# Kernel optimization log

Hardware: AMD Instinct MI355X
Metric: run time of the kernel (lower is better)

The kernel has to match this reference:

```python
import jax, jax.numpy as jnp
import numpy as np
from jax import lax

B, C, H, W = 2, 64, 48, 48
NH, DK, DV = 8, 64, 128          # heads, per-head d_k, per-head d_v
DN, NS, R = 128, 16, 4           # SS2D d_inner (expand=2), d_state, dt_rank
MULT = 4                          # FFN expansion
L = H * W


def layer_norm(x, w, b, eps=1e-5):
    m = x.mean(-1, keepdims=True)
    v = ((x - m) ** 2).mean(-1, keepdims=True)
    return (x - m) / jnp.sqrt(v + eps) * w + b


def conv2d(x, w, groups=1):
    # x: NCHW, w: OIHW
    return lax.conv_general_dilated(x, w, (1, 1), 'SAME',
                                    dimension_numbers=('NCHW', 'OIHW', 'NCHW'),
                                    feature_group_count=groups)


def setup_inputs() -> dict:
    key = jax.random.key(0)
    ks = jax.random.split(key, 24)
    rn = lambda k, shp, s=0.02: jax.random.normal(k, shp, jnp.float32) * s
    inp = {
        'enc_input': jax.random.normal(ks[0], (B, C, H, W), jnp.float32),
        'slf_attn_snr': jax.random.uniform(ks[1], (B, 1, H, W), jnp.float32),
        # MultiHeadAttention params
        'attn_wq': rn(ks[2], (C, NH * DK)),
        'attn_wk': rn(ks[3], (C, NH * DK)),
        'attn_wv': rn(ks[4], (C, NH * DV)),
        'attn_fc': rn(ks[5], (NH * DV, C)),
        'attn_ln_w': jnp.ones((C,), jnp.float32),
        'attn_ln_b': jnp.zeros((C,), jnp.float32),
        # SS2D params
        'ss_in_w': rn(ks[6], (C, 2 * DN)),
        'ss_conv_w': rn(ks[7], (DN, 1, 3, 3)),
        'ss_conv_b': jnp.zeros((DN,), jnp.float32),
        'ss_xproj_w': rn(ks[8], (4, R + 2 * NS, DN)),
        'ss_dt_w': rn(ks[9], (4, DN, R)),
        'ss_dt_b': rn(ks[10], (4, DN)),
        'ss_Alog': jnp.log(jnp.broadcast_to(jnp.arange(1, NS + 1, dtype=jnp.float32), (4, DN, NS))),
        'ss_D': jnp.ones((4, DN), jnp.float32),
        'ss_norm_w': jnp.ones((DN,), jnp.float32),
        'ss_norm_b': jnp.zeros((DN,), jnp.float32),
        'ss_out_w': rn(ks[11], (DN, C)),
        # FFN (PreNorm + conv block)
        'ffn_ln_w': jnp.ones((C,), jnp.float32),
        'ffn_ln_b': jnp.zeros((C,), jnp.float32),
        'ffn_w1': rn(ks[12], (C * MULT, C, 1, 1)),
        'ffn_dw': rn(ks[13], (C * MULT, 1, 3, 3)),
        'ffn_w2': rn(ks[14], (C, C * MULT, 1, 1)),
    }
    return inp


def reference(enc_input, slf_attn_snr, attn_wq, attn_wk, attn_wv, attn_fc,
              attn_ln_w, attn_ln_b, ss_in_w, ss_conv_w, ss_conv_b, ss_xproj_w,
              ss_dt_w, ss_dt_b, ss_Alog, ss_D, ss_norm_w, ss_norm_b, ss_out_w,
              ffn_ln_w, ffn_ln_b, ffn_w1, ffn_dw, ffn_w2):
    # ---- Multi-head self-attention over spatial tokens (SNR-biased) ----
    x_tok = enc_input.reshape(B, C, L).transpose(0, 2, 1)        # (B, L, C)
    q = (x_tok @ attn_wq).reshape(B, L, NH, DK).transpose(0, 2, 1, 3)
    k = (x_tok @ attn_wk).reshape(B, L, NH, DK).transpose(0, 2, 1, 3)
    v = (x_tok @ attn_wv).reshape(B, L, NH, DV).transpose(0, 2, 1, 3)
    scores = jnp.einsum('bhqd,bhkd->bhqk', q, k) / jnp.sqrt(jnp.float32(DK))
    snr_flat = slf_attn_snr.reshape(B, 1, 1, L)                  # bias over keys
    scores = scores + jnp.log(snr_flat + 1e-4)
    attn = jax.nn.softmax(scores, axis=-1)                       # (B, NH, L, L)
    o = jnp.einsum('bhqk,bhkd->bhqd', attn, v)
    o = o.transpose(0, 2, 1, 3).reshape(B, L, NH * DV) @ attn_fc
    enc_output = layer_norm(o + x_tok, attn_ln_w, attn_ln_b)     # post-LN residual
    enc_output = enc_output.transpose(0, 2, 1).reshape(B, C, H, W)

    # ---- SS2D: 4-direction 2D selective scan ----
    xh = enc_output.transpose(0, 2, 3, 1)                        # (B, H, W, C)
    snr_h = slf_attn_snr.transpose(0, 2, 3, 1)                   # (B, H, W, 1)
    xz = xh @ ss_in_w                                            # (B, H, W, 2*DN)
    x1, z = xz[..., :DN], xz[..., DN:]
    x1 = x1.transpose(0, 3, 1, 2)                                # (B, DN, H, W)
    x1 = conv2d(x1, ss_conv_w, groups=DN) + ss_conv_b[None, :, None, None]
    x1 = jax.nn.silu(x1)

    x_hw = x1.reshape(B, DN, L)
    x_wh = x1.transpose(0, 1, 3, 2).reshape(B, DN, L)
    xs = jnp.stack([x_hw, x_wh], axis=1)                         # (B, 2, DN, L)
    xs = jnp.concatenate([xs, jnp.flip(xs, axis=-1)], axis=1)    # (B, 4, DN, L)

    x_dbl = jnp.einsum('bkdl,kcd->bkcl', xs, ss_xproj_w)
    dts, Bs, Cs = x_dbl[:, :, :R], x_dbl[:, :, R:R + NS], x_dbl[:, :, R + NS:]
    dts = jnp.einsum('bkrl,kdr->bkdl', dts, ss_dt_w) + ss_dt_b[None, :, :, None]
    dts = jax.nn.softplus(dts)                                   # (B, 4, DN, L)
    A = -jnp.exp(ss_Alog)                                        # (4, DN, NS)

    def step(h, inp):
        xt, dtt, Bt, Ct = inp                                    # (B,4,DN),(B,4,DN),(B,4,NS),(B,4,NS)
        dA = jnp.exp(dtt[..., None] * A)                         # (B,4,DN,NS)
        h = h * dA + (dtt * xt)[..., None] * Bt[:, :, None, :]
        y = jnp.einsum('bkdn,bkn->bkd', h, Ct)
        return h, y

    h0 = jnp.zeros((B, 4, DN, NS), jnp.float32)
    elems = (xs.transpose(3, 0, 1, 2), dts.transpose(3, 0, 1, 2),
             Bs.transpose(3, 0, 1, 2), Cs.transpose(3, 0, 1, 2))
    _, ys = lax.scan(step, h0, elems)                            # (L, B, 4, DN)
    ys = ys.transpose(1, 2, 3, 0) + ss_D[None, :, :, None] * xs  # (B, 4, DN, L)

    inv = jnp.flip(ys[:, 2:4], axis=-1)                          # undo reversed scans
    wh = ys[:, 1].reshape(B, DN, W, H).transpose(0, 1, 3, 2).reshape(B, DN, L)
    invwh = inv[:, 1].reshape(B, DN, W, H).transpose(0, 1, 3, 2).reshape(B, DN, L)
    y = ys[:, 0] + inv[:, 0] + wh + invwh                        # (B, DN, L)
    y = y.transpose(0, 2, 1).reshape(B, H, W, DN)
    y = layer_norm(y, ss_norm_w, ss_norm_b) * jax.nn.silu(z) * snr_h
    x2 = y @ ss_out_w + enc_input.transpose(0, 2, 3, 1)          # (B, H, W, C)

    # ---- PreNorm conv FeedForward ----
    xn = layer_norm(x2, ffn_ln_w, ffn_ln_b).transpose(0, 3, 1, 2)
    h1 = jax.nn.gelu(conv2d(xn, ffn_w1), approximate=False)
    h1 = jax.nn.gelu(conv2d(h1, ffn_dw, groups=C * MULT), approximate=False)
    h1 = conv2d(h1, ffn_w2).transpose(0, 2, 3, 1)
    x3 = h1 + x2

    return x3.transpose(0, 3, 1, 2)                              # (B, C, H, W)
```

## Files before the change

### kernel.cpp

```cpp
#include <hip/hip_runtime.h>
#include <hip/hip_bf16.h>

#define Bq 2
#define Cc 64
#define Hh 48
#define Ww 48
#define Ll 2304
#define NHh 8
#define DKk 64
#define DVv 128
#define DNn 128
#define NSs 16
#define Rr 4
#define SCH 48
#define SNC 48
#define TT 8

#define OQ    0u
#define OK_   2359296u
#define OV    4718592u
#define OO    9437184u
#define OX2   15040512u
#define OVT   15630336u
#define WS_NEED_FLOATS (OVT + 4718592u)
#define ODT2  OQ
#define OYS2  OK_
#define OX1P  OV
#define OZ    (OV + 589824u)
#define OX1S  (OV + 1179648u)
#define OBS2  (OV + 1769472u)
#define OCS2  (OV + 2064384u)
#define OCSA  (OV + 2359296u)
#define OCSB  (OV + 3145728u)
#define OHST  (OV + 3932160u)
#define OH1A  OO
#define OH1B  (OO + 1179648u)

typedef short short8v __attribute__((ext_vector_type(8)));
typedef short short4v __attribute__((ext_vector_type(4)));
typedef float f32x4 __attribute__((ext_vector_type(4)));
typedef unsigned short ushort_t;

__device__ __forceinline__ float geluf(float x) {
  return 0.5f * x * (1.0f + erff(x * 0.70710678118654752f));
}
__device__ __forceinline__ float siluf(float x) {
  return x / (1.0f + __expf(-x));
}
__device__ __forceinline__ float softplusf(float x) {
  return fmaxf(x, 0.0f) + log1pf(__expf(-fabsf(x)));
}
__device__ __forceinline__ int spmap(int k, int l) {
  if (k == 0) return l;
  if (k == 1) return (l % 48) * 48 + l / 48;
  if (k == 2) return 2303 - l;
  int l2 = 2303 - l; return (l2 % 48) * 48 + l2 / 48;
}
__device__ __forceinline__ short f2bf(float f) {
  unsigned u = __float_as_uint(f);
  unsigned r = (u + 0x7FFFu + ((u >> 16) & 1u)) >> 16;
  return (short)r;
}

__global__ void k_code(float* out) { if (threadIdx.x == 0) out[0] = 25000.f; }

__global__ __launch_bounds__(256) void k_qkv(const float* __restrict__ enc,
    const float* __restrict__ wq, const float* __restrict__ wk,
    const float* __restrict__ wv, float* __restrict__ ws) {
  int l0 = blockIdx.x * TT; int b = blockIdx.y;
  int t = threadIdx.x;
  __shared__ float xs[64][12];
  {
    int idx = t, c = idx >> 3, i = idx & 7;
    xs[c][i] = enc[(size_t)b * Cc * Ll + (size_t)c * Ll + l0 + i];
    idx = t + 256; c = idx >> 3; i = idx & 7;
    xs[c][i] = enc[(size_t)b * Cc * Ll + (size_t)c * Ll + l0 + i];
  }
  __syncthreads();
  ushort_t* qb = (ushort_t*)(ws + OQ);
  ushort_t* kb = (ushort_t*)(ws + OK_);
  float* v = ws + OV;
#pragma unroll
  for (int g = 0; g < 6; ++g) {
    int j = t + g * 256;
    float acc[TT];
#pragma unroll
    for (int i = 0; i < TT; ++i) acc[i] = 0.f;
    const float* wp; int col, stride;
    if (j < 512) { wp = wq + j; stride = 512; col = j; }
    else if (j < 1024) { wp = wk + (j - 512); stride = 512; col = j - 512; }
    else { wp = wv + (j - 1024); stride = 1024; col = j - 1024; }
    for (int c = 0; c < 64; ++c) {
      float w = wp[(size_t)c * stride];
      const float4* xc = (const float4*)&xs[c][0];
      float4 x0 = xc[0], x1 = xc[1];
      acc[0] += x0.x * w; acc[1] += x0.y * w;
      acc[2] += x0.z * w; acc[3] += x0.w * w;
      acc[4] += x1.x * w; acc[5] += x1.y * w;
      acc[6] += x1.z * w; acc[7] += x1.w * w;
    }
    if (j < 512) {
#pragma unroll
      for (int i = 0; i < TT; ++i)
        qb[((size_t)(b * 8 + (col >> 6)) * Ll + l0 + i) * 64 + (col & 63)] =
            (ushort_t)f2bf(acc[i] * 0.125f);
    } else if (j < 1024) {
#pragma unroll
      for (int i = 0; i < TT; ++i)
        kb[((size_t)(b * 8 + (col >> 6)) * Ll + l0 + i) * 64 + (col & 63)] =
            (ushort_t)f2bf(acc[i]);
    } else {
#pragma unroll
      for (int i = 0; i < TT; ++i)
        v[((size_t)(b * 8 + (col >> 7)) * Ll + l0 + i) * 128 + (col & 127)] = acc[i];
    }
  }
}

__global__ __launch_bounds__(256) void k_vt(float* __restrict__ ws) {
  int bh = blockIdx.y;
  int l0 = blockIdx.x * 64;
  int t = threadIdx.x;
  __shared__ float tile[128][65];
  const float* vp = ws + OV + ((size_t)bh * Ll + l0) * 128;
  for (int i = t; i < 64 * 32; i += 256) {
    int l = i >> 5, dv4 = (i & 31) * 4;
    float4 a = *(const float4*)(vp + (size_t)l * 128 + dv4);
    tile[dv4][l] = a.x; tile[dv4 + 1][l] = a.y;
    tile[dv4 + 2][l] = a.z; tile[dv4 + 3][l] = a.w;
  }
  __syncthreads();
  ushort_t* vt = (ushort_t*)(ws + OVT) + (size_t)bh * 128 * Ll + l0;
  for (int i = t; i < 128 * 16; i += 256) {
    int dv = i >> 4, l4 = (i & 15) * 4;
    short4v a;
    a[0] = f2bf(tile[dv][l4]); a[1] = f2bf(tile[dv][l4 + 1]);
    a[2] = f2bf(tile[dv][l4 + 2]); a[3] = f2bf(tile[dv][l4 + 3]);
    *(short4v*)(vt + (size_t)dv * Ll + l4) = a;
  }
}

#define NKT 36
#define LSK 72
__global__ __launch_bounds__(256) void k_attn(const float* __restrict__ snr,
                                              float* __restrict__ ws) {
  int bh = blockIdx.y; int b = bh >> 3; int hd = bh & 7;
  int q0 = blockIdx.x * 64;
  int t = threadIdx.x;
  int w = t >> 6, lane = t & 63;
  int m16 = lane & 15, quad = lane >> 4;

  __shared__ __align__(16) ushort_t Ks[2][64 * LSK];
  __shared__ __align__(16) ushort_t Vs[2][128 * LSK];
  __shared__ __align__(16) ushort_t Ps[4 * 16 * LSK];
  __shared__ float sfac_s[2][64];
  __shared__ float lsc[4][16];

  const ushort_t* qbf = (const ushort_t*)(ws + OQ) + (size_t)bh * Ll * 64;
  const ushort_t* kbf = (const ushort_t*)(ws + OK_) + (size_t)bh * Ll * 64;
  const ushort_t* vtb = (const ushort_t*)(ws + OVT) + (size_t)bh * 128 * Ll;

  short8v qa[2];
  {
    const ushort_t* qrp = qbf + (size_t)(q0 + w * 16 + m16) * 64 + quad * 8;
    qa[0] = *(const short8v*)qrp;
    qa[1] = *(const short8v*)(qrp + 32);
  }
  int sk_key = t >> 2, sk_d0 = (t & 3) * 16;
  int sv_dv = t >> 1, sv_k0 = (t & 1) * 32;

  short8v kreg[2], vreg[4];
  float snr_reg = 0.f;
  {
    const ushort_t* ksrc = kbf + (size_t)sk_key * 64 + sk_d0;
    kreg[0] = *(const short8v*)ksrc;
    kreg[1] = *(const short8v*)(ksrc + 8);
    const ushort_t* vsrc = vtb + (size_t)sv_dv * Ll + sv_k0;
#pragma unroll
    for (int i = 0; i < 4; ++i) vreg[i] = *(const short8v*)(vsrc + i * 8);
    if (t < 64) snr_reg = snr[b * Ll + t];
  }

  f32x4 oacc[8];
#pragma unroll
  for (int i = 0; i < 8; ++i) oacc[i] = (f32x4)0.f;
  float l_r[4] = {0.f, 0.f, 0.f, 0.f};

  for (int kt = 0; kt < NKT; ++kt) {
    int buf = kt & 1;
    *(short8v*)&Ks[buf][sk_key * LSK + sk_d0] = kreg[0];
    *(short8v*)&Ks[buf][sk_key * LSK + sk_d0 + 8] = kreg[1];
#pragma unroll
    for (int i = 0; i < 4; ++i)
      *(short8v*)&Vs[buf][sv_dv * LSK + sv_k0 + i * 8] = vreg[i];
    if (t < 64) sfac_s[buf][t] = snr_reg + 1e-4f;
    __syncthreads();
    if (kt + 1 < NKT) {
      int k0n = (kt + 1) * 64;
      const ushort_t* ksrc = kbf + (size_t)(k0n + sk_key) * 64 + sk_d0;
      kreg[0] = *(const short8v*)ksrc;
      kreg[1] = *(const short8v*)(ksrc + 8);
      const ushort_t* vsrc = vtb + (size_t)sv_dv * Ll + k0n + sv_k0;
#pragma unroll
      for (int i = 0; i < 4; ++i) vreg[i] = *(const short8v*)(vsrc + i * 8);
      if (t < 64) snr_reg = snr[b * Ll + k0n + t];
    }

    f32x4 sac[4];
#pragma unroll
    for (int n = 0; n < 4; ++n) {
      int key = n * 16 + m16;
      short8v kb0 = *(const short8v*)&Ks[buf][key * LSK + quad * 8];
      short8v kb1 = *(const short8v*)&Ks[buf][key * LSK + 32 + quad * 8];
      f32x4 acc = (f32x4)0.f;
      acc = __builtin_amdgcn_mfma_f32_16x16x32_bf16(qa[0], kb0, acc, 0, 0, 0);
      acc = __builtin_amdgcn_mfma_f32_16x16x32_bf16(qa[1], kb1, acc, 0, 0, 0);
      sac[n] = acc;
    }
    float sf[4];
#pragma unroll
    for (int n = 0; n < 4; ++n) sf[n] = sfac_s[buf][n * 16 + m16];
    ushort_t* pw = &Ps[w * 16 * LSK];
#pragma unroll
    for (int r = 0; r < 4; ++r) {
#pragma unroll
      for (int n = 0; n < 4; ++n) {
        float p = __expf(sac[n][r]) * sf[n];
        l_r[r] += p;
        pw[(quad * 4 + r) * LSK + n * 16 + m16] = (ushort_t)f2bf(p);
      }
    }
    short8v pb0 = *(const short8v*)&pw[m16 * LSK + quad * 8];
    short8v pb1 = *(const short8v*)&pw[m16 * LSK + 32 + quad * 8];
#pragma unroll
    for (int dt_ = 0; dt_ < 8; ++dt_) {
      const ushort_t* vrow = &Vs[buf][(dt_ * 16 + m16) * LSK];
      short8v va0 = *(const short8v*)&vrow[quad * 8];
      short8v va1 = *(const short8v*)&vrow[32 + quad * 8];
      f32x4 o = oacc[dt_];
      o = __builtin_amdgcn_mfma_f32_16x16x32_bf16(va0, pb0, o, 0, 0, 0);
      o = __builtin_amdgcn_mfma_f32_16x16x32_bf16(va1, pb1, o, 0, 0, 0);
      oacc[dt_] = o;
    }
  }
#pragma unroll
  for (int r = 0; r < 4; ++r) {
    float lv = l_r[r];
    lv += __shfl_xor(lv, 1, 64);
    lv += __shfl_xor(lv, 2, 64);
    lv += __shfl_xor(lv, 4, 64);
    lv += __shfl_xor(lv, 8, 64);
    l_r[r] = lv;
  }
  if (m16 == 0) {
#pragma unroll
    for (int r = 0; r < 4; ++r) lsc[w][quad * 4 + r] = l_r[r];
  }
  __builtin_amdgcn_s_waitcnt(0);
  float linv = 1.f / lsc[w][m16];
  float* op = ws + OO + ((size_t)(b * Ll + q0 + w * 16 + m16)) * 1024 + hd * 128;
#pragma unroll
  for (int dt_ = 0; dt_ < 8; ++dt_) {
#pragma unroll
    for (int r = 0; r < 4; ++r) {
      op[dt_ * 16 + quad * 4 + r] = oacc[dt_][r] * linv;
    }
  }
}

__global__ __launch_bounds__(256) void k_oprojxz(const float* __restrict__ enc,
    const float* __restrict__ fc, const float* __restrict__ lnw,
    const float* __restrict__ lnb, const float* __restrict__ ssin,
    float* __restrict__ ws) {
  int l0 = blockIdx.x * TT, b = blockIdx.y, t = threadIdx.x;
  __shared__ float orow[1024][9];
  __shared__ float part[4][TT][64];
  __shared__ float xh_s[64][9];
  const float* op = ws + OO + ((size_t)(b * Ll + l0)) * 1024;
#pragma unroll
  for (int k = 0; k < 4; ++k) {
    int c = t + k * 256;
#pragma unroll
    for (int i = 0; i < TT; ++i) orow[c][i] = op[(size_t)i * 1024 + c];
  }
  __syncthreads();
  int col = t & 63, seg = t >> 6;
  {
    float acc[TT];
#pragma unroll
    for (int i = 0; i < TT; ++i) acc[i] = 0.f;
    const float* fcs = fc + (size_t)(seg * 256) * 64 + col;
    for (int c = 0; c < 256; ++c) {
      float w = fcs[(size_t)c * 64];
      const float* orc = &orow[seg * 256 + c][0];
#pragma unroll
      for (int i = 0; i < TT; ++i) acc[i] += orc[i] * w;
    }
#pragma unroll
    for (int i = 0; i < TT; ++i) part[seg][i][col] = acc[i];
  }
  __syncthreads();
  if (t < 64) {
    float lw = lnw[t], lb = lnb[t];
#pragma unroll
    for (int i = 0; i < TT; ++i) {
      float a = part[0][i][t] + part[1][i][t] + part[2][i][t] + part[3][i][t];
      a += enc[(size_t)b * Cc * Ll + (size_t)t * Ll + l0 + i];
      float s = a;
#pragma unroll
      for (int o = 32; o >= 1; o >>= 1) s += __shfl_xor(s, o, 64);
      float m = s * (1.f / 64.f);
      float dd = a - m;
      float vs = dd * dd;
#pragma unroll
      for (int o = 32; o >= 1; o >>= 1) vs += __shfl_xor(vs, o, 64);
      xh_s[t][i] = dd * rsqrtf(vs * (1.f / 64.f) + 1e-5f) * lw + lb;
    }
  }
  __syncthreads();
  {
    float acc2[TT];
#pragma unroll
    for (int i = 0; i < TT; ++i) acc2[i] = 0.f;
    for (int c = 0; c < 64; ++c) {
      float w = ssin[c * 256 + t];
      const float* xc = &xh_s[c][0];
#pragma unroll
      for (int i = 0; i < TT; ++i) acc2[i] += xc[i] * w;
    }
    if (t < 128) {
#pragma unroll
      for (int i = 0; i < TT; ++i)
        ws[OX1P + ((size_t)(b * Ll + l0 + i)) * 128 + t] = acc2[i];
    } else {
#pragma unroll
      for (int i = 0; i < TT; ++i)
        ws[OZ + ((size_t)(b * Ll + l0 + i)) * 128 + (t - 128)] = acc2[i];
    }
  }
}

__global__ __launch_bounds__(256) void k_conv(const float* __restrict__ cw,
    const float* __restrict__ cb, float* __restrict__ ws) {
  int l0 = blockIdx.x * TT, b = blockIdx.y, t = threadIdx.x;
  int h = l0 / 48, w0 = l0 % 48;
  __shared__ float tile[3][10][128];
  for (int idx = t; idx < 3840; idx += 256) {
    int r = idx / 1280, rem = idx % 1280;
    int col = rem >> 7, d = rem & 127;
    int hh = h + r - 1, wx = w0 + col - 1;
    float v = 0.f;
    if (hh >= 0 && hh < 48 && wx >= 0 && wx < 48)
      v = ws[OX1P + ((size_t)(b * Ll + hh * 48 + wx)) * 128 + d];
    tile[r][col][d] = v;
  }
  __syncthreads();
  int d = t & 127, half = t >> 7;
  float cwr[9];
#pragma unroll
  for (int j = 0; j < 9; ++j) cwr[j] = cw[d * 9 + j];
  float cbv = cb[d];
#pragma unroll
  for (int j = 0; j < 4; ++j) {
    int i = half * 4 + j;
    float acc = cbv;
#pragma unroll
    for (int kh = 0; kh < 3; ++kh)
#pragma unroll
      for (int kw = 0; kw < 3; ++kw)
        acc += tile[kh][i + kw][d] * cwr[kh * 3 + kw];
    ws[OX1S + ((size_t)(b * Ll + l0 + i)) * 128 + d] = siluf(acc);
  }
}

__global__ __launch_bounds__(128) void k_xdbl(const float* __restrict__ xw,
    const float* __restrict__ dtw, const float* __restrict__ dtb,
    float* __restrict__ ws) {
  int l0 = blockIdx.x * TT;
  int by = blockIdx.y; int b = by >> 2; int k = by & 3;
  int t = threadIdx.x;
  __shared__ float xv[128][9];
  __shared__ float pr[36][TT];
#pragma unroll
  for (int i = 0; i < TT; ++i) {
    int sp = spmap(k, l0 + i);
    xv[t][i] = ws[OX1S + ((size_t)(b * Ll) + sp) * 128 + t];
  }
  __syncthreads();
  if (t < 36) {
    float s[TT];
#pragma unroll
    for (int i = 0; i < TT; ++i) s[i] = 0.f;
    const float* wp = xw + (size_t)(k * 36 + t) * 128;
    for (int d = 0; d < 128; ++d) {
      float w = wp[d];
      const float* xc = &xv[d][0];
#pragma unroll
      for (int i = 0; i < TT; ++i) s[i] += xc[i] * w;
    }
#pragma unroll
    for (int i = 0; i < TT; ++i) pr[t][i] = s[i];
  }
  __syncthreads();
  {
    int d = t;
    const float* wp = dtw + (size_t)(k * 128 + d) * 4;
    float w0 = wp[0], w1 = wp[1], w2 = wp[2], w3 = wp[3];
    float bb = dtb[k * 128 + d];
#pragma unroll
    for (int i = 0; i < TT; ++i) {
      float v = pr[0][i] * w0 + pr[1][i] * w1 + pr[2][i] * w2 + pr[3][i] * w3 + bb;
      ws[ODT2 + ((size_t)(by * Ll + l0 + i)) * 128 + d] = softplusf(v);
    }
  }
  if (t < 16) {
#pragma unroll
    for (int i = 0; i < TT; ++i)
      ws[OBS2 + ((size_t)(by * Ll + l0 + i)) * 16 + t] = pr[4 + t][i];
  } else if (t < 32) {
#pragma unroll
    for (int i = 0; i < TT; ++i)
      ws[OCS2 + ((size_t)(by * Ll + l0 + i)) * 16 + (t - 16)] = pr[20 + (t - 16)][i];
  }
}

__global__ __launch_bounds__(256) void k_scanA(const float* __restrict__ alog,
                                               float* __restrict__ ws) {
  int c = blockIdx.x;
  int bk = blockIdx.y;
  int b = bk >> 2, k = bk & 3;
  int t = threadIdx.x;
  int n = t & 15, dg = t >> 4;
  __shared__ float dt_s[2][128], x_s[2][128], Bs_s[2][16];
  float A_r[8], ap[8], bc[8];
#pragma unroll
  for (int i = 0; i < 8; ++i) {
    int d = dg * 8 + i;
    A_r[i] = -__expf(alog[(size_t)((k * 128 + d) * 16) + n]);
    ap[i] = 1.f; bc[i] = 0.f;
  }
  const float* dtp = ws + ODT2 + ((size_t)bk * Ll) * 128;
  const float* bsp = ws + OBS2 + ((size_t)bk * Ll) * 16;
  const float* xb = ws + OX1S + (size_t)b * Ll * 128;
  float r_a = 0.f, r_Bs = 0.f;
  {
    int l = c * SCH;
    int sp = spmap(k, l);
    if (t < 128) r_a = dtp[(size_t)l * 128 + t];
    else r_a = xb[(size_t)sp * 128 + (t - 128)];
    if (t < 16) r_Bs = bsp[(size_t)l * 16 + t];
  }
  for (int ll = 0; ll < SCH; ++ll) {
    int buf = ll & 1;
    if (t < 128) dt_s[buf][t] = r_a;
    else x_s[buf][t - 128] = r_a;
    if (t < 16) Bs_s[buf][t] = r_Bs;
    __syncthreads();
    if (ll + 1 < SCH) {
      int l2 = c * SCH + ll + 1;
      int sp2 = spmap(k, l2);
      if (t < 128) r_a = dtp[(size_t)l2 * 128 + t];
      else r_a = xb[(size_t)sp2 * 128 + (t - 128)];
      if (t < 16) r_Bs = bsp[(size_t)l2 * 16 + t];
    }
    float Bv = Bs_s[buf][n];
#pragma unroll
    for (int i = 0; i < 8; ++i) {
      int d = dg * 8 + i;
      float dtv = dt_s[buf][d];
      float a = __expf(dtv * A_r[i]);
      bc[i] = bc[i] * a + dtv * x_s[buf][d] * Bv;
      ap[i] *= a;
    }
  }
  float* csa = ws + OCSA + ((size_t)(bk * SNC + c) * 128) * 16;
  float* csb = ws + OCSB + ((size_t)(bk * SNC + c) * 128) * 16;
#pragma unroll
  for (int i = 0; i < 8; ++i) {
    int d = dg * 8 + i;
    csa[d * 16 + n] = ap[i];
    csb[d * 16 + n] = bc[i];
  }
}

__global__ __launch_bounds__(256) void k_scanB(float* __restrict__ ws) {
  int g = blockIdx.x * 256 + threadIdx.x;
  int bk = g >> 11;
  int dn = g & 2047;
  const float* csa = ws + OCSA;
  const float* csb = ws + OCSB;
  float* hst = ws + OHST;
  size_t base = (size_t)bk * SNC * 2048 + dn;
  float h = 0.f;
  float a = csa[base], bq = csb[base];
  for (int c = 0; c < SNC; ++c) {
    float na = 0.f, nb = 0.f;
    if (c + 1 < SNC) {
      size_t idx2 = base + (size_t)(c + 1) * 2048;
      na = csa[idx2]; nb = csb[idx2];
    }
    hst[base + (size_t)c * 2048] = h;
    h = a * h + bq;
    a = na; bq = nb;
  }
}

__global__ __launch_bounds__(256) void k_scanC(const float* __restrict__ alog,
    const float* __restrict__ Dp, float* __restrict__ ws) {
  int c = blockIdx.x, bk = blockIdx.y;
  int b = bk >> 2, k = bk & 3;
  int t = threadIdx.x;
  int n = t & 15, dg = t >> 4;
  __shared__ float dt_s[2][128], x_s[2][128], Bs_s[2][16], Cs_s[2][16];
  float A_r[8], h[8], Dv[8];
#pragma unroll
  for (int i = 0; i < 8; ++i) {
    int d = dg * 8 + i;
    A_r[i] = -__expf(alog[(size_t)((k * 128 + d) * 16) + n]);
    h[i] = ws[OHST + ((size_t)(bk * SNC + c) * 128 + d) * 16 + n];
    Dv[i] = Dp[k * 128 + d];
  }
  const float* dtp = ws + ODT2 + ((size_t)bk * Ll) * 128;
  const float* bsp = ws + OBS2 + ((size_t)bk * Ll) * 16;
  const float* csp = ws + OCS2 + ((size_t)bk * Ll) * 16;
  const float* xb = ws + OX1S + (size_t)b * Ll * 128;
  float* yp = ws + OYS2 + ((size_t)bk * Ll) * 128;
  float r_a = 0.f, r_bc = 0.f;
  {
    int l = c * SCH;
    int sp = spmap(k, l);
    if (t < 128) r_a = dtp[(size_t)l * 128 + t];
    else r_a = xb[(size_t)sp * 128 + (t - 128)];
    if (t < 16) r_bc = bsp[(size_t)l * 16 + t];
    else if (t < 32) r_bc = csp[(size_t)l * 16 + (t - 16)];
  }
  for (int ll = 0; ll < SCH; ++ll) {
    int buf = ll & 1;
    if (t < 128) dt_s[buf][t] = r_a;
    else x_s[buf][t - 128] = r_a;
    if (t < 16) Bs_s[buf][t] = r_bc;
    else if (t < 32) Cs_s[buf][t - 16] = r_bc;
    __syncthreads();
    if (ll + 1 < SCH) {
      int l2 = c * SCH + ll + 1;
      int sp2 = spmap(k, l2);
      if (t < 128) r_a = dtp[(size_t)l2 * 128 + t];
      else r_a = xb[(size_t)sp2 * 128 + (t - 128)];
      if (t < 16) r_bc = bsp[(size_t)l2 * 16 + t];
      else if (t < 32) r_bc = csp[(size_t)l2 * 16 + (t - 16)];
    }
    int l = c * SCH + ll;
    float Bv = Bs_s[buf][n], Cv = Cs_s[buf][n];
    float yacc[8];
#pragma unroll
    for (int i = 0; i < 8; ++i) {
      int d = dg * 8 + i;
      float dtv = dt_s[buf][d];
      float a = __expf(dtv * A_r[i]);
      h[i] = h[i] * a + dtv * x_s[buf][d] * Bv;
      yacc[i] = h[i] * Cv;
    }
#pragma unroll
    for (int i = 0; i < 8; ++i) {
      float yv = yacc[i];
      yv += __shfl_xor(yv, 1, 64);
      yv += __shfl_xor(yv, 2, 64);
      yv += __shfl_xor(yv, 4, 64);
      yv += __shfl_xor(yv, 8, 64);
      yacc[i] = yv;
    }
    if (n == 0) {
#pragma unroll
      for (int i = 0; i < 8; ++i) {
        int d = dg * 8 + i;
        yp[(size_t)l * 128 + d] = yacc[i] + Dv[i] * x_s[buf][d];
      }
    }
  }
}

__global__ __launch_bounds__(256) void k_combffn1(const float* __restrict__ enc,
    const float* __restrict__ nw, const float* __restrict__ nb,
    const float* __restrict__ snr, const float* __restrict__ ow,
    const float* __restrict__ lw, const float* __restrict__ lb,
    const float* __restrict__ w1, float* __restrict__ ws) {
  int l0 = blockIdx.x * TT, b = blockIdx.y, t = threadIdx.x;
  __shared__ float yr[128][9];
  __shared__ float redm[2][TT], redq[2][TT];
  __shared__ float part[2][TT][64];
  __shared__ float xn_s[64][9];
  int lane = t & 63, wid = (t >> 6) & 1;
  float v[TT], m[TT];
  if (t < 128) {
    int d = t;
    const float* ysb = ws + OYS2;
#pragma unroll
    for (int i = 0; i < TT; ++i) {
      int l = l0 + i;
      int hh = l / 48, wwp = l % 48;
      int lT = wwp * 48 + hh;
      v[i] = ysb[((size_t)(b * 4 + 0) * Ll + l) * 128 + d] +
             ysb[((size_t)(b * 4 + 2) * Ll + (2303 - l)) * 128 + d] +
             ysb[((size_t)(b * 4 + 1) * Ll + lT) * 128 + d] +
             ysb[((size_t)(b * 4 + 3) * Ll + (2303 - lT)) * 128 + d];
    }
    float s[TT];
#pragma unroll
    for (int i = 0; i < TT; ++i) s[i] = v[i];
#pragma unroll
    for (int o = 32; o >= 1; o >>= 1)
#pragma unroll
      for (int i = 0; i < TT; ++i) s[i] += __shfl_xor(s[i], o, 64);
    if (lane == 0) {
#pragma unroll
      for (int i = 0; i < TT; ++i) redm[wid][i] = s[i];
    }
  }
  __syncthreads();
  if (t < 128) {
    float q[TT];
#pragma unroll
    for (int i = 0; i < TT; ++i) {
      m[i] = (redm[0][i] + redm[1][i]) * (1.f / 128.f);
      float dv = v[i] - m[i];
      q[i] = dv * dv;
    }
#pragma unroll
    for (int o = 32; o >= 1; o >>= 1)
#pragma unroll
      for (int i = 0; i < TT; ++i) q[i] += __shfl_xor(q[i], o, 64);
    if (lane == 0) {
#pragma unroll
      for (int i = 0; i < TT; ++i) redq[wid][i] = q[i];
    }
  }
  __syncthreads();
  if (t < 128) {
    int d = t;
    float nwv = nw[d], nbv = nb[d];
#pragma unroll
    for (int i = 0; i < TT; ++i) {
      int l = l0 + i;
      float var = (redq[0][i] + redq[1][i]) * (1.f / 128.f);
      float y = (v[i] - m[i]) * rsqrtf(var + 1e-5f) * nwv + nbv;
      float zv = ws[OZ + ((size_t)(b * Ll + l)) * 128 + d];
      y *= siluf(zv);
      y *= snr[b * Ll + l];
      yr[d][i] = y;
    }
  }
  __syncthreads();
  if (t < 128) {
    int col = t & 63, seg = t >> 6;
    float acc[TT];
#pragma unroll
    for (int i = 0; i < TT; ++i) acc[i] = 0.f;
    const float* ows = ow + (size_t)(seg * 64) * 64 + col;
    for (int c = 0; c < 64; ++c) {
      float w = ows[c * 64];
      const float* yc = &yr[seg * 64 + c][0];
#pragma unroll
      for (int i = 0; i < TT; ++i) acc[i] += yc[i] * w;
    }
#pragma unroll
    for (int i = 0; i < TT; ++i) part[seg][i][col] = acc[i];
  }
  __syncthreads();
  if (t < 64) {
    float lwv = lw[t], lbv = lb[t];
#pragma unroll
    for (int i = 0; i < TT; ++i) {
      float a = part[0][i][t] + part[1][i][t];
      a += enc[(size_t)b * Cc * Ll + (size_t)t * Ll + l0 + i];
      ws[OX2 + ((size_t)(b * Ll + l0 + i)) * 64 + t] = a;
      float s = a;
#pragma unroll
      for (int o = 32; o >= 1; o >>= 1) s += __shfl_xor(s, o, 64);
      float mm = s * (1.f / 64.f);
      float dd2 = a - mm;
      float vs = dd2 * dd2;
#pragma unroll
      for (int o = 32; o >= 1; o >>= 1) vs += __shfl_xor(vs, o, 64);
      xn_s[t][i] = dd2 * rsqrtf(vs * (1.f / 64.f) + 1e-5f) * lwv + lbv;
    }
  }
  __syncthreads();
  {
    float acc2[TT];
#pragma unroll
    for (int i = 0; i < TT; ++i) acc2[i] = 0.f;
    const float* wp = w1 + (size_t)t * 64;
    for (int c = 0; c < 64; ++c) {
      float w = wp[c];
      const float* xc = &xn_s[c][0];
#pragma unroll
      for (int i = 0; i < TT; ++i) acc2[i] += xc[i] * w;
    }
#pragma unroll
    for (int i = 0; i < TT; ++i)
      ws[OH1A + ((size_t)(b * Ll + l0 + i)) * 256 + t] = geluf(acc2[i]);
  }
}

__global__ __launch_bounds__(256) void k_ffndw(const float* __restrict__ dww,
                                               float* __restrict__ ws) {
  int l0 = blockIdx.x * TT, b = blockIdx.y, t = threadIdx.x;
  int h = l0 / 48, w0 = l0 % 48;
  __shared__ float tile[3][10][256];
  for (int idx = t; idx < 7680; idx += 256) {
    int r = idx / 2560, rem = idx % 2560;
    int col = rem >> 8, ch = rem & 255;
    int hh = h + r - 1, wx = w0 + col - 1;
    float v = 0.f;
    if (hh >= 0 && hh < 48 && wx >= 0 && wx < 48)
      v = ws[OH1A + ((size_t)(b * Ll + hh * 48 + wx)) * 256 + ch];
    tile[r][col][ch] = v;
  }
  __syncthreads();
  float dwr[9];
#pragma unroll
  for (int j = 0; j < 9; ++j) dwr[j] = dww[t * 9 + j];
#pragma unroll
  for (int i = 0; i < TT; ++i) {
    float acc = 0.f;
#pragma unroll
    for (int kh = 0; kh < 3; ++kh)
#pragma unroll
      for (int kw = 0; kw < 3; ++kw)
        acc += tile[kh][i + kw][t] * dwr[kh * 3 + kw];
    ws[OH1B + ((size_t)(b * Ll + l0 + i)) * 256 + t] = geluf(acc);
  }
}

__global__ __launch_bounds__(256) void k_ffn2(const float* __restrict__ w2,
                                              float* __restrict__ ws,
                                              float* __restrict__ out) {
  int l0 = blockIdx.x * TT, b = blockIdx.y, t = threadIdx.x;
  __shared__ float hr[256][9];
  __shared__ float part[4][TT][64];
  const float* hp = ws + OH1B + ((size_t)(b * Ll + l0)) * 256;
#pragma unroll
  for (int i = 0; i < TT; ++i) hr[t][i] = hp[(size_t)i * 256 + t];
  __syncthreads();
  int col = t & 63, seg = t >> 6;
  {
    float acc[TT];
#pragma unroll
    for (int i = 0; i < TT; ++i) acc[i] = 0.f;
    const float* wp = w2 + (size_t)col * 256 + seg * 64;
    for (int c = 0; c < 64; ++c) {
      float w = wp[c];
      const float* hc = &hr[seg * 64 + c][0];
#pragma unroll
      for (int i = 0; i < TT; ++i) acc[i] += hc[i] * w;
    }
#pragma unroll
    for (int i = 0; i < TT; ++i) part[seg][i][col] = acc[i];
  }
  __syncthreads();
  if (t < 64) {
    float av[TT];
#pragma unroll
    for (int i = 0; i < TT; ++i) {
      float a = part[0][i][t] + part[1][i][t] + part[2][i][t] + part[3][i][t];
      av[i] = a + ws[OX2 + ((size_t)(b * Ll + l0 + i)) * 64 + t];
    }
    float* opx = out + ((size_t)(b * 64 + t)) * 2304 + l0;
    *(float4*)opx = make_float4(av[0], av[1], av[2], av[3]);
    *((float4*)opx + 1) = make_float4(av[4], av[5], av[6], av[7]);
  }
}

extern "C" void kernel_launch(void* const* d_in, const int* in_sizes, int n_in,
                              void* d_out, int out_size, void* d_ws, size_t ws_size,
                              hipStream_t stream) {
  (void)in_sizes; (void)n_in; (void)out_size;
  const float* enc  = (const float*)d_in[0];
  const float* snr  = (const float*)d_in[1];
  const float* wq   = (const float*)d_in[2];
  const float* wk   = (const float*)d_in[3];
  const float* wv   = (const float*)d_in[4];
  const float* fc   = (const float*)d_in[5];
  const float* alnw = (const float*)d_in[6];
  const float* alnb = (const float*)d_in[7];
  const float* ssin = (const float*)d_in[8];
  const float* cw   = (const float*)d_in[9];
  const float* cb   = (const float*)d_in[10];
  const float* xw   = (const float*)d_in[11];
  const float* dtw  = (const float*)d_in[12];
  const float* dtb  = (const float*)d_in[13];
  const float* alog = (const float*)d_in[14];
  const float* Dp   = (const float*)d_in[15];
  const float* nw   = (const float*)d_in[16];
  const float* nb   = (const float*)d_in[17];
  const float* ow   = (const float*)d_in[18];
  const float* flnw = (const float*)d_in[19];
  const float* flnb = (const float*)d_in[20];
  const float* w1   = (const float*)d_in[21];
  const float* dww  = (const float*)d_in[22];
  const float* w2   = (const float*)d_in[23];
  float* ws = (float*)d_ws;
  float* out = (float*)d_out;

  if (ws_size < (size_t)WS_NEED_FLOATS * 4) {
    hipLaunchKernelGGL(k_code, dim3(1), dim3(64), 0, stream, out);
    return;
  }

  hipLaunchKernelGGL(k_qkv, dim3(Ll / TT, Bq), dim3(256), 0, stream, enc, wq, wk, wv, ws);
  hipLaunchKernelGGL(k_vt, dim3(Ll / 64, Bq * NHh), dim3(256), 0, stream, ws);
  hipLaunchKernelGGL(k_attn, dim3(Ll / 64, Bq * NHh), dim3(256), 0, stream, snr, ws);
  hipLaunchKernelGGL(k_oprojxz, dim3(Ll / TT, Bq), dim3(256), 0, stream, enc, fc, alnw, alnb, ssin, ws);
  hipLaunchKernelGGL(k_conv, dim3(Ll / TT, Bq), dim3(256), 0, stream, cw, cb, ws);
  hipLaunchKernelGGL(k_xdbl, dim3(Ll / TT, Bq * 4), dim3(128), 0, stream, xw, dtw, dtb, ws);
  hipLaunchKernelGGL(k_scanA, dim3(SNC, Bq * 4), dim3(256), 0, stream, alog, ws);
  hipLaunchKernelGGL(k_scanB, dim3(64), dim3(256), 0, stream, ws);
  hipLaunchKernelGGL(k_scanC, dim3(SNC, Bq * 4), dim3(256), 0, stream, alog, Dp, ws);
  hipLaunchKernelGGL(k_combffn1, dim3(Ll / TT, Bq), dim3(256), 0, stream, enc, nw, nb, snr, ow, flnw, flnb, w1, ws);
  hipLaunchKernelGGL(k_ffndw, dim3(Ll / TT, Bq), dim3(256), 0, stream, dww, ws);
  hipLaunchKernelGGL(k_ffn2, dim3(Ll / TT, Bq), dim3(256), 0, stream, w2, ws, out);
}
```

Before: 444.6 us.

## Split attention key range across two blocks and combine partial outputs

The attention kernel now splits the key dimension in two (split-K, flash-decoding style). Each half writes unnormalized output and row sums to separate workspace regions. A new combine kernel adds the two halves and normalizes. This doubles the grid from 576 to 1152 blocks to fill more compute units, and drops the double-buffered LDS so each block uses less shared memory. The cost is an extra full-size fp32 output write and read, an extra kernel launch, and an extra barrier per key tile because the single LDS buffer has to be protected.

New measurement: 433.7 us. 2.5% less time.

```diff
diff --git a/kernel.cpp b/kernel.cpp
--- a/kernel.cpp
+++ b/kernel.cpp
@@ -20,6 +20,7 @@
 #define OK_   2359296u
 #define OV    4718592u
 #define OO    9437184u
+#define OLP   14450688u
 #define OX2   15040512u
 #define OVT   15630336u
 #define WS_NEED_FLOATS (OVT + 4718592u)
@@ -140,21 +141,22 @@
   }
 }
 
-#define NKT 36
+#define NKT2 18
 #define LSK 72
 __global__ __launch_bounds__(256) void k_attn(const float* __restrict__ snr,
                                               float* __restrict__ ws) {
   int bh = blockIdx.y; int b = bh >> 3; int hd = bh & 7;
   int q0 = blockIdx.x * 64;
+  int ks = blockIdx.z;
+  int kbase = ks * (Ll / 2);
   int t = threadIdx.x;
   int w = t >> 6, lane = t & 63;
   int m16 = lane & 15, quad = lane >> 4;
 
-  __shared__ __align__(16) ushort_t Ks[2][64 * LSK];
-  __shared__ __align__(16) ushort_t Vs[2][128 * LSK];
+  __shared__ __align__(16) ushort_t Ks[64 * LSK];
+  __shared__ __align__(16) ushort_t Vs[128 * LSK];
   __shared__ __align__(16) ushort_t Ps[4 * 16 * LSK];
-  __shared__ float sfac_s[2][64];
-  __shared__ float lsc[4][16];
+  __shared__ float sfac_s[64];
 
   const ushort_t* qbf = (const ushort_t*)(ws + OQ) + (size_t)bh * Ll * 64;
   const ushort_t* kbf = (const ushort_t*)(ws + OK_) + (size_t)bh * Ll * 64;
@@ -172,13 +174,13 @@
   short8v kreg[2], vreg[4];
   float snr_reg = 0.f;
   {
-    const ushort_t* ksrc = kbf + (size_t)sk_key * 64 + sk_d0;
+    const ushort_t* ksrc = kbf + (size_t)(kbase + sk_key) * 64 + sk_d0;
     kreg[0] = *(const short8v*)ksrc;
     kreg[1] = *(const short8v*)(ksrc + 8);
-    const ushort_t* vsrc = vtb + (size_t)sv_dv * Ll + sv_k0;
+    const ushort_t* vsrc = vtb + (size_t)sv_dv * Ll + kbase + sv_k0;
 #pragma unroll
     for (int i = 0; i < 4; ++i) vreg[i] = *(const short8v*)(vsrc + i * 8);
-    if (t < 64) snr_reg = snr[b * Ll + t];
+    if (t < 64) snr_reg = snr[b * Ll + kbase + t];
   }
 
   f32x4 oacc[8];
@@ -186,17 +188,17 @@
   for (int i = 0; i < 8; ++i) oacc[i] = (f32x4)0.f;
   float l_r[4] = {0.f, 0.f, 0.f, 0.f};
 
-  for (int kt = 0; kt < NKT; ++kt) {
-    int buf = kt & 1;
-    *(short8v*)&Ks[buf][sk_key * LSK + sk_d0] = kreg[0];
-    *(short8v*)&Ks[buf][sk_key * LSK + sk_d0 + 8] = kreg[1];
+  for (int kt = 0; kt < NKT2; ++kt) {
+    __syncthreads();
+    *(short8v*)&Ks[sk_key * LSK + sk_d0] = kreg[0];
+    *(short8v*)&Ks[sk_key * LSK + sk_d0 + 8] = kreg[1];
 #pragma unroll
     for (int i = 0; i < 4; ++i)
-      *(short8v*)&Vs[buf][sv_dv * LSK + sv_k0 + i * 8] = vreg[i];
-    if (t < 64) sfac_s[buf][t] = snr_reg + 1e-4f;
+      *(short8v*)&Vs[sv_dv * LSK + sv_k0 + i * 8] = vreg[i];
+    if (t < 64) sfac_s[t] = snr_reg + 1e-4f;
     __syncthreads();
-    if (kt + 1 < NKT) {
-      int k0n = (kt + 1) * 64;
+    if (kt + 1 < NKT2) {
+      int k0n = kbase + (kt + 1) * 64;
       const ushort_t* ksrc = kbf + (size_t)(k0n + sk_key) * 64 + sk_d0;
       kreg[0] = *(const short8v*)ksrc;
       kreg[1] = *(const short8v*)(ksrc + 8);
@@ -210,8 +212,8 @@
 #pragma unroll
     for (int n = 0; n < 4; ++n) {
       int key = n * 16 + m16;
-      short8v kb0 = *(const short8v*)&Ks[buf][key * LSK + quad * 8];
-      short8v kb1 = *(const short8v*)&Ks[buf][key * LSK + 32 + quad * 8];
+      short8v kb0 = *(const short8v*)&Ks[key * LSK + quad * 8];
+      short8v kb1 = *(const short8v*)&Ks[key * LSK + 32 + quad * 8];
       f32x4 acc = (f32x4)0.f;
       acc = __builtin_amdgcn_mfma_f32_16x16x32_bf16(qa[0], kb0, acc, 0, 0, 0);
       acc = __builtin_amdgcn_mfma_f32_16x16x32_bf16(qa[1], kb1, acc, 0, 0, 0);
@@ -219,7 +221,7 @@
     }
     float sf[4];
 #pragma unroll
-    for (int n = 0; n < 4; ++n) sf[n] = sfac_s[buf][n * 16 + m16];
+    for (int n = 0; n < 4; ++n) sf[n] = sfac_s[n * 16 + m16];
     ushort_t* pw = &Ps[w * 16 * LSK];
 #pragma unroll
     for (int r = 0; r < 4; ++r) {
@@ -234,7 +236,7 @@
     short8v pb1 = *(const short8v*)&pw[m16 * LSK + 32 + quad * 8];
 #pragma unroll
     for (int dt_ = 0; dt_ < 8; ++dt_) {
-      const ushort_t* vrow = &Vs[buf][(dt_ * 16 + m16) * LSK];
+      const ushort_t* vrow = &Vs[(dt_ * 16 + m16) * LSK];
       short8v va0 = *(const short8v*)&vrow[quad * 8];
       short8v va1 = *(const short8v*)&vrow[32 + quad * 8];
       f32x4 o = oacc[dt_];
@@ -253,19 +255,39 @@
     l_r[r] = lv;
   }
   if (m16 == 0) {
-#pragma unroll
-    for (int r = 0; r < 4; ++r) lsc[w][quad * 4 + r] = l_r[r];
-  }
-  __builtin_amdgcn_s_waitcnt(0);
-  float linv = 1.f / lsc[w][m16];
-  float* op = ws + OO + ((size_t)(b * Ll + q0 + w * 16 + m16)) * 1024 + hd * 128;
+    float* lp = ws + OLP + (size_t)ks * (Bq * NHh * Ll) + (size_t)bh * Ll;
+#pragma unroll
+    for (int r = 0; r < 4; ++r) lp[q0 + w * 16 + quad * 4 + r] = l_r[r];
+  }
+  float* opb = ws + (ks ? OV : OO);
+  float* op = opb + ((size_t)(b * Ll + q0 + w * 16 + m16)) * 1024 + hd * 128;
 #pragma unroll
   for (int dt_ = 0; dt_ < 8; ++dt_) {
 #pragma unroll
     for (int r = 0; r < 4; ++r) {
-      op[dt_ * 16 + quad * 4 + r] = oacc[dt_][r] * linv;
-    }
-  }
+      op[dt_ * 16 + quad * 4 + r] = oacc[dt_][r];
+    }
+  }
+}
+
+__global__ __launch_bounds__(256) void k_ocomb(float* __restrict__ ws) {
+  size_t e4 = (size_t)blockIdx.x * 256 + threadIdx.x;
+  int c4 = (int)(e4 & 255);
+  size_t bl = e4 >> 8;
+  int b = (int)(bl / Ll), l = (int)(bl % Ll);
+  int hd = c4 >> 5;
+  int bh = b * 8 + hd;
+  float l1 = ws[OLP + (size_t)bh * Ll + l];
+  float l2 = ws[OLP + (size_t)(Bq * NHh * Ll) + (size_t)bh * Ll + l];
+  float linv = 1.f / (l1 + l2);
+  float4* po = (float4*)(ws + OO) + e4;
+  const float4* pv = (const float4*)(ws + OV) + e4;
+  float4 a = *po, bq = *pv;
+  a.x = (a.x + bq.x) * linv;
+  a.y = (a.y + bq.y) * linv;
+  a.z = (a.z + bq.z) * linv;
+  a.w = (a.w + bq.w) * linv;
+  *po = a;
 }
 
 __global__ __launch_bounds__(256) void k_oprojxz(const float* __restrict__ enc,
@@ -809,7 +831,8 @@
 
   hipLaunchKernelGGL(k_qkv, dim3(Ll / TT, Bq), dim3(256), 0, stream, enc, wq, wk, wv, ws);
   hipLaunchKernelGGL(k_vt, dim3(Ll / 64, Bq * NHh), dim3(256), 0, stream, ws);
-  hipLaunchKernelGGL(k_attn, dim3(Ll / 64, Bq * NHh), dim3(256), 0, stream, snr, ws);
+  hipLaunchKernelGGL(k_attn, dim3(Ll / 64, Bq * NHh, 2), dim3(256), 0, stream, snr, ws);
+  hipLaunchKernelGGL(k_ocomb, dim3(Bq * Ll, 1), dim3(256), 0, stream, ws);
   hipLaunchKernelGGL(k_oprojxz, dim3(Ll / TT, Bq), dim3(256), 0, stream, enc, fc, alnw, alnb, ssin, ws);
   hipLaunchKernelGGL(k_conv, dim3(Ll / TT, Bq), dim3(256), 0, stream, cw, cb, ws);
   hipLaunchKernelGGL(k_xdbl, dim3(Ll / TT, Bq * 4), dim3(128), 0, stream, xw, dtw, dtb, ws);
```
